# Kernel tuning notes

Measured on AMD Instinct MI355X. Metric: run time of the kernel, lower is better.

Reference implementation:

```python
import jax, jax.numpy as jnp
import numpy as np

N, E, F_IN, H, EDIM, L, OUT = 100000, 1600000, 256, 128, 16, 3, 64


def setup_inputs() -> dict:
    key = jax.random.key(0)
    ks = jax.random.split(key, 12)
    s = lambda k, shape: jax.random.normal(k, shape, jnp.float32) * 0.05
    return dict(
        x=jax.random.normal(ks[0], (N, F_IN), jnp.float32),
        edge_index=jax.random.randint(ks[1], (2, E), 0, N, jnp.int32),
        edge_attr=jax.random.normal(ks[2], (E, EDIM), jnp.float32),
        in_w=s(ks[3], (F_IN, H)), in_b=jnp.zeros((H,), jnp.float32),
        Wk=s(ks[4], (L, H, H)), bk=jnp.zeros((L, H), jnp.float32),
        Wq=s(ks[5], (L, H, H)), bq=jnp.zeros((L, H), jnp.float32),
        Wv=s(ks[6], (L, H, H)), bv=jnp.zeros((L, H), jnp.float32),
        We=s(ks[7], (L, EDIM, H)), be=jnp.zeros((L, H), jnp.float32),
        Ws=s(ks[8], (L, H, H)), bs=jnp.zeros((L, H), jnp.float32),
        ln_g=jnp.ones((L, H), jnp.float32), ln_b=jnp.zeros((L, H), jnp.float32),
        out_w=s(ks[9], (H, OUT)),
    )


def _layernorm(x, g, b, eps=1e-5):
    mu = x.mean(-1, keepdims=True)
    var = ((x - mu) ** 2).mean(-1, keepdims=True)
    return (x - mu) * jax.lax.rsqrt(var + eps) * g + b


def reference(x, edge_index, edge_attr, in_w, in_b, Wk, bk, Wq, bq, Wv, bv,
              We, be, Ws, bs, ln_g, ln_b, out_w):
    src, dst = edge_index[0], edge_index[1]  # j (source), i (target)
    h = x @ in_w + in_b                      # in_proj; dropout_prob=0 -> identity
    n = h.shape[0]
    n_layers = Wk.shape[0]
    for l in range(n_layers):
        # ResGatedGraphConv: out_i = W_skip x_i + sum_j sigmoid(k_i + e_ij + q_j) * v_j
        k = h @ Wk[l] + bk[l]                # keys on targets  [N,H]
        q = h @ Wq[l] + bq[l]                # queries on sources [N,H]
        v = h @ Wv[l] + bv[l]                # values on sources [N,H]
        e = edge_attr @ We[l] + be[l]        # edge embedding [E,H]
        gate = jax.nn.sigmoid(k[dst] + e + q[src])   # [E,H]
        msg = gate * v[src]                  # [E,H]
        agg = jax.ops.segment_sum(msg, dst, num_segments=n)  # scatter-add [N,H]
        h = agg + (h @ Ws[l] + bs[l])        # root/skip term
        h = jax.nn.gelu(_layernorm(h, ln_g[l], ln_b[l]), approximate=False)
    return h @ out_w                          # out_proj (bias=False)
```

## Files before the change

kernel.cpp:

```cpp
#include <hip/hip_runtime.h>
#include <hip/hip_fp16.h>
#include <cmath>

#define Nn   100000
#define Ee   1600000
#define FIN  256
#define Hh   128
#define EDIMM 16
#define NL   3
#define NOUT 64

typedef _Float16 f16x8 __attribute__((ext_vector_type(8)));
typedef float f32x4 __attribute__((ext_vector_type(4)));

static __device__ __forceinline__ __half2 u2h2(unsigned int u) {
  union { unsigned int u; __half2 h; } c; c.u = u; return c.h;
}
static __device__ __forceinline__ unsigned int h22u(__half2 h) {
  union { unsigned int u; __half2 h; } c; c.h = h; return c.u;
}

__global__ __launch_bounds__(128) void in_proj_kernel(const float* __restrict__ x,
    const float* __restrict__ w, const float* __restrict__ b, __half* __restrict__ h) {
  __shared__ float xs[8][FIN];
  int r0 = blockIdx.x * 8;
  for (int i = threadIdx.x; i < 8 * FIN; i += 128) {
    int r = i >> 8, c = i & (FIN - 1);
    int rr = r0 + r;
    xs[r][c] = (rr < Nn) ? x[rr * FIN + c] : 0.f;
  }
  __syncthreads();
  int t = threadIdx.x;
  float acc[8] = {};
  for (int kk = 0; kk < FIN; kk++) {
    float wv = w[kk * Hh + t];
#pragma unroll
    for (int r = 0; r < 8; r++) acc[r] += xs[r][kk] * wv;
  }
  float bias = b[t];
#pragma unroll
  for (int r = 0; r < 8; r++) {
    int rr = r0 + r;
    if (rr < Nn) h[rr * Hh + t] = __float2half(acc[r] + bias);
  }
}

__global__ __launch_bounds__(256) void prep_weights_kernel(const float* __restrict__ Wk,
    const float* __restrict__ Wq, const float* __restrict__ Wv, const float* __restrict__ Ws,
    __half* __restrict__ WtT) {
  int mat = blockIdx.x, l = blockIdx.y;
  const float* W = (mat == 0 ? Wk : mat == 1 ? Wq : mat == 2 ? Wv : Ws) + (size_t)l * Hh * Hh;
  __half* out = WtT + ((size_t)(l * 4 + mat)) * Hh * Hh;
  for (int i = threadIdx.x; i < Hh * Hh; i += 256) {
    int k = i >> 7, n = i & 127;
    out[(size_t)n * Hh + k] = __float2half(W[i]);
  }
}

__global__ __launch_bounds__(256) void kqvs_mfma_kernel(
    const __half* __restrict__ h, const __half* __restrict__ WtT_l,
    const float* __restrict__ bk, const float* __restrict__ bq,
    const float* __restrict__ bv, const float* __restrict__ bs,
    __half* __restrict__ kb, __half* __restrict__ qvj, __half* __restrict__ hnew) {
  __shared__ __half Wl[128][136];
  __shared__ __half Ht[32][136];
  int mat = blockIdx.x;
  int r0 = blockIdx.y * 32;
  int tid = threadIdx.x;

  const uint4* wg = (const uint4*)(WtT_l + (size_t)mat * Hh * Hh);
  for (int i = tid; i < 2048; i += 256) {
    int rw = i >> 4, cw = i & 15;
    *(uint4*)(&Wl[rw][cw * 8]) = wg[i];
  }
  const uint4* hg = (const uint4*)(h + (size_t)r0 * Hh);
  for (int i = tid; i < 512; i += 256) {
    int rh = i >> 4, ch = i & 15;
    *(uint4*)(&Ht[rh][ch * 8]) = hg[i];
  }
  __syncthreads();

  int wv = tid >> 6, lane = tid & 63;
  int rowHalf = wv & 1, colHalf = wv >> 1;
  int quad = lane >> 4, l16 = lane & 15;

  f32x4 acc[4];
#pragma unroll
  for (int t = 0; t < 4; t++) acc[t] = (f32x4){0.f, 0.f, 0.f, 0.f};

#pragma unroll
  for (int kstep = 0; kstep < 4; kstep++) {
    f16x8 afrag = *(const f16x8*)(&Ht[rowHalf * 16 + l16][kstep * 32 + quad * 8]);
#pragma unroll
    for (int t = 0; t < 4; t++) {
      int n = colHalf * 64 + t * 16 + l16;
      f16x8 bfrag = *(const f16x8*)(&Wl[n][kstep * 32 + quad * 8]);
      acc[t] = __builtin_amdgcn_mfma_f32_16x16x32_f16(afrag, bfrag, acc[t], 0, 0, 0);
    }
  }

  const float* bp = (mat == 0) ? bk : (mat == 1) ? bq : (mat == 2) ? bv : bs;
#pragma unroll
  for (int t = 0; t < 4; t++) {
    int col = colHalf * 64 + t * 16 + l16;
    float bval = bp[col];
#pragma unroll
    for (int r = 0; r < 4; r++) {
      int row = r0 + rowHalf * 16 + quad * 4 + r;
      __half hv = __float2half(acc[t][r] + bval);
      if (mat == 0)       kb[(size_t)row * Hh + col] = hv;
      else if (mat == 1)  qvj[(size_t)row * 256 + (col >> 1) * 4 + (col & 1)] = hv;
      else if (mat == 2)  qvj[(size_t)row * 256 + (col >> 1) * 4 + 2 + (col & 1)] = hv;
      else                hnew[(size_t)row * Hh + col] = hv;
    }
  }
}

__global__ __launch_bounds__(256) void zero_kernel(int* __restrict__ p, int n) {
  int i = blockIdx.x * 256 + threadIdx.x;
  if (i < n) p[i] = 0;
}

__global__ __launch_bounds__(256) void hist_kernel(const int* __restrict__ ei_dst,
                                                   int* __restrict__ counts) {
  int e = blockIdx.x * 256 + threadIdx.x;
  if (e < Ee) atomicAdd(&counts[ei_dst[e]], 1);
}

__global__ __launch_bounds__(256) void scan_block_kernel(const int* __restrict__ counts,
    int* __restrict__ rowptr, int* __restrict__ bsums) {
  __shared__ int tsums[256];
  int b = blockIdx.x, t = threadIdx.x;
  int base = b * 1024 + t * 4;
  int v[4]; int s = 0;
#pragma unroll
  for (int j = 0; j < 4; j++) {
    int idx = base + j;
    v[j] = (idx < Nn) ? counts[idx] : 0;
    s += v[j];
  }
  tsums[t] = s;
  __syncthreads();
  for (int off = 1; off < 256; off <<= 1) {
    int y = (t >= off) ? tsums[t - off] : 0;
    __syncthreads();
    tsums[t] += y;
    __syncthreads();
  }
  int excl = tsums[t] - s;
#pragma unroll
  for (int j = 0; j < 4; j++) {
    int idx = base + j;
    if (idx < Nn) rowptr[idx] = excl;
    excl += v[j];
  }
  if (t == 255) bsums[b] = tsums[255];
}

__global__ __launch_bounds__(128) void scan_sums_kernel(int* __restrict__ bsums, int nb) {
  __shared__ int sh[128];
  int t = threadIdx.x;
  int v = (t < nb) ? bsums[t] : 0;
  sh[t] = v;
  __syncthreads();
  for (int off = 1; off < 128; off <<= 1) {
    int y = (t >= off) ? sh[t - off] : 0;
    __syncthreads();
    sh[t] += y;
    __syncthreads();
  }
  if (t < nb) bsums[t] = sh[t] - v;
}

__global__ __launch_bounds__(256) void finalize_rowptr_kernel(int* __restrict__ rowptr,
    const int* __restrict__ bsums, int* __restrict__ cursor) {
  int i = blockIdx.x * 256 + threadIdx.x;
  if (i < Nn) {
    int r = rowptr[i] + bsums[i >> 10];
    rowptr[i] = r;
    cursor[i] = r;
  }
  if (i == Nn) rowptr[Nn] = Ee;
}

__global__ __launch_bounds__(256) void fill_perm_kernel(const int* __restrict__ ei_src,
    const int* __restrict__ ei_dst, const float* __restrict__ ea,
    int* __restrict__ cursor, int* __restrict__ src_perm,
    unsigned int* __restrict__ ea_perm) {
  int e = blockIdx.x * 256 + threadIdx.x;
  if (e < Ee) {
    int d = ei_dst[e];
    int slot = atomicAdd(&cursor[d], 1);
    src_perm[slot] = ei_src[e];
    const float4* s = (const float4*)(ea + (size_t)e * EDIMM);
    float4 f[4] = { s[0], s[1], s[2], s[3] };
    unsigned int u[16];
#pragma unroll
    for (int j = 0; j < 4; j++) {
      u[j*4+0] = h22u(__half2half2(__float2half(f[j].x)));
      u[j*4+1] = h22u(__half2half2(__float2half(f[j].y)));
      u[j*4+2] = h22u(__half2half2(__float2half(f[j].z)));
      u[j*4+3] = h22u(__half2half2(__float2half(f[j].w)));
    }
    uint4* dp = (uint4*)(ea_perm + (size_t)slot * EDIMM);
#pragma unroll
    for (int j = 0; j < 4; j++)
      dp[j] = make_uint4(u[j*4+0], u[j*4+1], u[j*4+2], u[j*4+3]);
  }
}

#define EA_CAP 48
__global__ __launch_bounds__(256, 8) void edge_csr_kernel(
    const __half* __restrict__ kb, const __half* __restrict__ qvj,
    const int* __restrict__ src_perm, const unsigned int* __restrict__ ea_perm,
    const int* __restrict__ rowptr,
    const float* __restrict__ We_l, const float* __restrict__ be_l,
    const float* __restrict__ ln_g_l, const float* __restrict__ ln_b_l,
    __half* __restrict__ hbuf) {
  __shared__ uint4 lds_ea[4][EA_CAP * 4];
  int wave = threadIdx.x >> 6;
  int lane = threadIdx.x & 63;
  int row = blockIdx.x * 4 + wave;
  int c0 = lane * 2;

  __half2 wpk[EDIMM];
#pragma unroll
  for (int d = 0; d < EDIMM; d++) {
    float2 wv = *(const float2*)(We_l + d * Hh + c0);
    wpk[d] = __floats2half2_rn(wv.x, wv.y);
  }
  float2 bef = *(const float2*)(be_l + c0);
  __half2 bev = __floats2half2_rn(bef.x, bef.y);

  __half2 kpk = *(const __half2*)(kb + (size_t)row * Hh + c0);
  __half2 kbev = __hadd2(kpk, bev);

  float agg0 = 0.f, agg1 = 0.f;
  int beg = rowptr[row], end = rowptr[row + 1];
  int deg = end - beg;
  int nl = (deg < EA_CAP) ? deg : EA_CAP;

  char* lbase = (char*)&lds_ea[wave][0];
  {
    int row_bytes = nl << 6;
    const char* gsrc = (const char*)(ea_perm + (size_t)beg * EDIMM);
    for (int c = 0; c < row_bytes; c += 1024) {
      int o = c + lane * 16;
      if (o < row_bytes) {
        __builtin_amdgcn_global_load_lds(
            (__attribute__((address_space(1))) void*)(gsrc + o),
            (__attribute__((address_space(3))) void*)(lbase + c),
            16, 0, 0);
      }
    }
  }

  const char* qvb = (const char*)qvj;
  unsigned loff = (unsigned)(lane << 3);

  auto edge_math = [&](uint4 a0, uint4 a1, uint4 a2, uint4 a3, uint2 qv) {
    __half2 qh = u2h2(qv.x), vh = u2h2(qv.y);
    __half2 acc = kbev;
    acc = __hfma2(u2h2(a0.x), wpk[0],  acc);
    acc = __hfma2(u2h2(a0.y), wpk[1],  acc);
    acc = __hfma2(u2h2(a0.z), wpk[2],  acc);
    acc = __hfma2(u2h2(a0.w), wpk[3],  acc);
    acc = __hfma2(u2h2(a1.x), wpk[4],  acc);
    acc = __hfma2(u2h2(a1.y), wpk[5],  acc);
    acc = __hfma2(u2h2(a1.z), wpk[6],  acc);
    acc = __hfma2(u2h2(a1.w), wpk[7],  acc);
    acc = __hfma2(u2h2(a2.x), wpk[8],  acc);
    acc = __hfma2(u2h2(a2.y), wpk[9],  acc);
    acc = __hfma2(u2h2(a2.z), wpk[10], acc);
    acc = __hfma2(u2h2(a2.w), wpk[11], acc);
    acc = __hfma2(u2h2(a3.x), wpk[12], acc);
    acc = __hfma2(u2h2(a3.y), wpk[13], acc);
    acc = __hfma2(u2h2(a3.z), wpk[14], acc);
    acc = __hfma2(u2h2(a3.w), wpk[15], acc);
    __half2 pre = __hadd2(acc, qh);
    float p0 = __half2float(__low2half(pre));
    float p1 = __half2float(__high2half(pre));
    float g0 = __builtin_amdgcn_rcpf(1.f + __expf(-p0));
    float g1 = __builtin_amdgcn_rcpf(1.f + __expf(-p1));
    agg0 += g0 * __half2float(__low2half(vh));
    agg1 += g1 * __half2float(__high2half(vh));
  };

  {
    int nf = nl & ~3;
    int e = 0;
    uint2 qA0, qA1, qA2, qA3;
    if (nf) {
      int4 s4 = *(const int4*)(src_perm + beg);
      qA0 = *(const uint2*)(qvb + (((unsigned)s4.x << 9) + loff));
      qA1 = *(const uint2*)(qvb + (((unsigned)s4.y << 9) + loff));
      qA2 = *(const uint2*)(qvb + (((unsigned)s4.z << 9) + loff));
      qA3 = *(const uint2*)(qvb + (((unsigned)s4.w << 9) + loff));
    }
    asm volatile("s_waitcnt vmcnt(0)" ::: "memory");

    for (; e + 8 <= nf; e += 4) {
      int4 s4n = *(const int4*)(src_perm + beg + e + 4);
      uint2 qB0 = *(const uint2*)(qvb + (((unsigned)s4n.x << 9) + loff));
      uint2 qB1 = *(const uint2*)(qvb + (((unsigned)s4n.y << 9) + loff));
      uint2 qB2 = *(const uint2*)(qvb + (((unsigned)s4n.z << 9) + loff));
      uint2 qB3 = *(const uint2*)(qvb + (((unsigned)s4n.w << 9) + loff));
      const uint4* ee = (const uint4*)(lbase + (e << 6));
      edge_math(ee[0],  ee[1],  ee[2],  ee[3],  qA0);
      edge_math(ee[4],  ee[5],  ee[6],  ee[7],  qA1);
      edge_math(ee[8],  ee[9],  ee[10], ee[11], qA2);
      edge_math(ee[12], ee[13], ee[14], ee[15], qA3);
      qA0 = qB0; qA1 = qB1; qA2 = qB2; qA3 = qB3;
    }
    if (nf) {
      const uint4* ee = (const uint4*)(lbase + (e << 6));
      edge_math(ee[0],  ee[1],  ee[2],  ee[3],  qA0);
      edge_math(ee[4],  ee[5],  ee[6],  ee[7],  qA1);
      edge_math(ee[8],  ee[9],  ee[10], ee[11], qA2);
      edge_math(ee[12], ee[13], ee[14], ee[15], qA3);
      e += 4;
    }
    for (; e < nl; e++) {
      int src = src_perm[beg + e];
      uint2 qv = *(const uint2*)(qvb + (((unsigned)src << 9) + loff));
      const uint4* ee = (const uint4*)(lbase + (e << 6));
      edge_math(ee[0], ee[1], ee[2], ee[3], qv);
    }
    for (int eg = beg + nl; eg < end; eg++) {
      int src = src_perm[eg];
      const uint4* eb = (const uint4*)(ea_perm + (size_t)eg * EDIMM);
      uint4 a0 = eb[0], a1 = eb[1], a2 = eb[2], a3 = eb[3];
      uint2 qv = *(const uint2*)(qvb + (((unsigned)src << 9) + loff));
      edge_math(a0, a1, a2, a3, qv);
    }
  }

  __half2 hv2 = *(const __half2*)(hbuf + (size_t)row * Hh + c0);
  float y0 = __half2float(hv2.x) + agg0, y1 = __half2float(hv2.y) + agg1;
  float s = y0 + y1;
#pragma unroll
  for (int off = 32; off; off >>= 1) s += __shfl_xor(s, off);
  float mu = s * (1.f / 128.f);
  float d0 = y0 - mu, d1 = y1 - mu;
  float vv = d0 * d0 + d1 * d1;
#pragma unroll
  for (int off = 32; off; off >>= 1) vv += __shfl_xor(vv, off);
  float rstd = rsqrtf(vv * (1.f / 128.f) + 1e-5f);
  float2 lg = *(const float2*)(ln_g_l + c0);
  float2 lb = *(const float2*)(ln_b_l + c0);
  float o0 = d0 * rstd * lg.x + lb.x;
  float o1 = d1 * rstd * lg.y + lb.y;
  o0 = 0.5f * o0 * (1.f + erff(o0 * 0.70710678118654752f));
  o1 = 0.5f * o1 * (1.f + erff(o1 * 0.70710678118654752f));
  *(__half2*)(hbuf + (size_t)row * Hh + c0) = __floats2half2_rn(o0, o1);
}

__global__ __launch_bounds__(64) void out_proj_kernel(const __half* __restrict__ h,
    const float* __restrict__ w, float* __restrict__ out) {
  __shared__ float hs[16][Hh];
  int r0 = blockIdx.x * 16;
  const uint4* hg = (const uint4*)(h + (size_t)r0 * Hh);
  for (int i = threadIdx.x; i < 256; i += 64) {
    uint4 u = hg[i];
    int r = i >> 4, c = (i & 15) * 8;
    __half2 ha = u2h2(u.x), hb = u2h2(u.y), hc = u2h2(u.z), hd = u2h2(u.w);
    hs[r][c+0] = __half2float(ha.x); hs[r][c+1] = __half2float(ha.y);
    hs[r][c+2] = __half2float(hb.x); hs[r][c+3] = __half2float(hb.y);
    hs[r][c+4] = __half2float(hc.x); hs[r][c+5] = __half2float(hc.y);
    hs[r][c+6] = __half2float(hd.x); hs[r][c+7] = __half2float(hd.y);
  }
  __syncthreads();
  int t = threadIdx.x;
  float acc[16] = {};
  for (int kk = 0; kk < Hh; kk++) {
    float wv = w[kk * NOUT + t];
#pragma unroll
    for (int r = 0; r < 16; r++) acc[r] += hs[r][kk] * wv;
  }
#pragma unroll
  for (int r = 0; r < 16; r++) out[(size_t)(r0 + r) * NOUT + t] = acc[r];
}

extern "C" void kernel_launch(void* const* d_in, const int* in_sizes, int n_in,
                              void* d_out, int out_size, void* d_ws, size_t ws_size,
                              hipStream_t stream) {
  const float* x    = (const float*)d_in[0];
  const int*   ei   = (const int*)d_in[1];
  const float* ea   = (const float*)d_in[2];
  const float* in_w = (const float*)d_in[3];
  const float* in_b = (const float*)d_in[4];
  const float* Wk   = (const float*)d_in[5];
  const float* bk   = (const float*)d_in[6];
  const float* Wq   = (const float*)d_in[7];
  const float* bq   = (const float*)d_in[8];
  const float* Wv   = (const float*)d_in[9];
  const float* bv   = (const float*)d_in[10];
  const float* We   = (const float*)d_in[11];
  const float* be   = (const float*)d_in[12];
  const float* Ws   = (const float*)d_in[13];
  const float* bs   = (const float*)d_in[14];
  const float* ln_g = (const float*)d_in[15];
  const float* ln_b = (const float*)d_in[16];
  const float* out_w = (const float*)d_in[17];
  float* out = (float*)d_out;

  const int* ei_src = ei;
  const int* ei_dst = ei + Ee;

  size_t NH = (size_t)Nn * Hh;
  char* wsp = (char*)d_ws;
  __half* hA = (__half*)wsp;          wsp += NH * 2;
  __half* hB = (__half*)wsp;          wsp += NH * 2;
  __half* kb = (__half*)wsp;          wsp += NH * 2;
  __half* qvj = (__half*)wsp;         wsp += NH * 2 * 2;
  __half* WtT = (__half*)wsp;         wsp += (size_t)NL * 4 * Hh * Hh * 2;
  int* rowptr = (int*)wsp;            wsp += (Nn + 1) * 4;
  int* cursor = (int*)wsp;            wsp += Nn * 4;
  int* bsums  = (int*)wsp;            wsp += 128 * 4;
  int* src_perm = (int*)wsp;          wsp += (size_t)Ee * 4;
  unsigned int* ea_perm = (unsigned int*)wsp; wsp += (size_t)Ee * EDIMM * 4;

  const int NB_SCAN = (Nn + 1023) / 1024;

  zero_kernel<<<(Nn + 255) / 256, 256, 0, stream>>>(cursor, Nn);
  hist_kernel<<<(Ee + 255) / 256, 256, 0, stream>>>(ei_dst, cursor);
  scan_block_kernel<<<NB_SCAN, 256, 0, stream>>>(cursor, rowptr, bsums);
  scan_sums_kernel<<<1, 128, 0, stream>>>(bsums, NB_SCAN);
  finalize_rowptr_kernel<<<(Nn + 1 + 255) / 256, 256, 0, stream>>>(rowptr, bsums, cursor);
  fill_perm_kernel<<<(Ee + 255) / 256, 256, 0, stream>>>(ei_src, ei_dst, ea, cursor,
                                                         src_perm, ea_perm);
  prep_weights_kernel<<<dim3(4, NL), 256, 0, stream>>>(Wk, Wq, Wv, Ws, WtT);

  in_proj_kernel<<<(Nn + 7) / 8, 128, 0, stream>>>(x, in_w, in_b, hA);

  __half* h  = hA;
  __half* hn = hB;
  for (int l = 0; l < NL; l++) {
    kqvs_mfma_kernel<<<dim3(4, Nn / 32), 256, 0, stream>>>(h,
        WtT + (size_t)l * 4 * Hh * Hh,
        bk + l * Hh, bq + l * Hh, bv + l * Hh, bs + l * Hh,
        kb, qvj, hn);
    edge_csr_kernel<<<Nn / 4, 256, 0, stream>>>(kb, qvj, src_perm, ea_perm,
        rowptr, We + l * EDIMM * Hh, be + l * Hh,
        ln_g + l * Hh, ln_b + l * Hh, hn);
    __half* tmp = h; h = hn; hn = tmp;
  }

  out_proj_kernel<<<Nn / 16, 64, 0, stream>>>(h, out_w, out);
}
```

Measured before the change: 1.336 ms.

## Pack edge attributes as plain half2 and fold log2e into gate weights

```diff
diff --git a/kernel.cpp b/kernel.cpp
--- a/kernel.cpp
+++ b/kernel.cpp
@@ -9,6 +9,7 @@
 #define EDIMM 16
 #define NL   3
 #define NOUT 64
+#define LOG2E 1.4426950408889634f
 
 typedef _Float16 f16x8 __attribute__((ext_vector_type(8)));
 typedef float f32x4 __attribute__((ext_vector_type(4)));
@@ -19,6 +20,13 @@
 static __device__ __forceinline__ unsigned int h22u(__half2 h) {
   union { unsigned int u; __half2 h; } c; c.h = h; return c.u;
 }
+
+#define PK_FMA_LO(acc, a, w) \
+  asm("v_pk_fma_f16 %0, %1, %2, %0 op_sel:[0,0,0] op_sel_hi:[0,1,1]" \
+      : "+v"(acc) : "v"(a), "v"(w))
+#define PK_FMA_HI(acc, a, w) \
+  asm("v_pk_fma_f16 %0, %1, %2, %0 op_sel:[1,0,0] op_sel_hi:[1,1,1]" \
+      : "+v"(acc) : "v"(a), "v"(w))
 
 __global__ __launch_bounds__(128) void in_proj_kernel(const float* __restrict__ x,
     const float* __restrict__ w, const float* __restrict__ b, __half* __restrict__ h) {
@@ -50,10 +58,11 @@
     __half* __restrict__ WtT) {
   int mat = blockIdx.x, l = blockIdx.y;
   const float* W = (mat == 0 ? Wk : mat == 1 ? Wq : mat == 2 ? Wv : Ws) + (size_t)l * Hh * Hh;
+  float sc = (mat < 2) ? LOG2E : 1.f;
   __half* out = WtT + ((size_t)(l * 4 + mat)) * Hh * Hh;
   for (int i = threadIdx.x; i < Hh * Hh; i += 256) {
     int k = i >> 7, n = i & 127;
-    out[(size_t)n * Hh + k] = __float2half(W[i]);
+    out[(size_t)n * Hh + k] = __float2half(W[i] * sc);
   }
 }
 
@@ -100,10 +109,11 @@
   }
 
   const float* bp = (mat == 0) ? bk : (mat == 1) ? bq : (mat == 2) ? bv : bs;
+  float bscale = (mat < 2) ? LOG2E : 1.f;
 #pragma unroll
   for (int t = 0; t < 4; t++) {
     int col = colHalf * 64 + t * 16 + l16;
-    float bval = bp[col];
+    float bval = bp[col] * bscale;
 #pragma unroll
     for (int r = 0; r < 4; r++) {
       int row = r0 + rowHalf * 16 + quad * 4 + r;
@@ -193,47 +203,40 @@
     int slot = atomicAdd(&cursor[d], 1);
     src_perm[slot] = ei_src[e];
     const float4* s = (const float4*)(ea + (size_t)e * EDIMM);
-    float4 f[4] = { s[0], s[1], s[2], s[3] };
-    unsigned int u[16];
-#pragma unroll
-    for (int j = 0; j < 4; j++) {
-      u[j*4+0] = h22u(__half2half2(__float2half(f[j].x)));
-      u[j*4+1] = h22u(__half2half2(__float2half(f[j].y)));
-      u[j*4+2] = h22u(__half2half2(__float2half(f[j].z)));
-      u[j*4+3] = h22u(__half2half2(__float2half(f[j].w)));
-    }
-    uint4* dp = (uint4*)(ea_perm + (size_t)slot * EDIMM);
-#pragma unroll
-    for (int j = 0; j < 4; j++)
-      dp[j] = make_uint4(u[j*4+0], u[j*4+1], u[j*4+2], u[j*4+3]);
+    float4 f0 = s[0], f1 = s[1], f2 = s[2], f3 = s[3];
+    uint4* dp = (uint4*)(ea_perm + (size_t)slot * 8);
+    dp[0] = make_uint4(h22u(__floats2half2_rn(f0.x, f0.y)), h22u(__floats2half2_rn(f0.z, f0.w)),
+                       h22u(__floats2half2_rn(f1.x, f1.y)), h22u(__floats2half2_rn(f1.z, f1.w)));
+    dp[1] = make_uint4(h22u(__floats2half2_rn(f2.x, f2.y)), h22u(__floats2half2_rn(f2.z, f2.w)),
+                       h22u(__floats2half2_rn(f3.x, f3.y)), h22u(__floats2half2_rn(f3.z, f3.w)));
   }
 }
 
 #define EA_CAP 48
-__global__ __launch_bounds__(256, 8) void edge_csr_kernel(
+__global__ __launch_bounds__(256, 6) void edge_csr_kernel(
     const __half* __restrict__ kb, const __half* __restrict__ qvj,
     const int* __restrict__ src_perm, const unsigned int* __restrict__ ea_perm,
     const int* __restrict__ rowptr,
     const float* __restrict__ We_l, const float* __restrict__ be_l,
     const float* __restrict__ ln_g_l, const float* __restrict__ ln_b_l,
     __half* __restrict__ hbuf) {
-  __shared__ uint4 lds_ea[4][EA_CAP * 4];
+  __shared__ uint4 lds_ea[4][EA_CAP * 2];
   int wave = threadIdx.x >> 6;
   int lane = threadIdx.x & 63;
   int row = blockIdx.x * 4 + wave;
   int c0 = lane * 2;
 
-  __half2 wpk[EDIMM];
+  unsigned wpk[EDIMM];
 #pragma unroll
   for (int d = 0; d < EDIMM; d++) {
     float2 wv = *(const float2*)(We_l + d * Hh + c0);
-    wpk[d] = __floats2half2_rn(wv.x, wv.y);
+    wpk[d] = h22u(__floats2half2_rn(wv.x * LOG2E, wv.y * LOG2E));
   }
   float2 bef = *(const float2*)(be_l + c0);
-  __half2 bev = __floats2half2_rn(bef.x, bef.y);
+  __half2 bev = __floats2half2_rn(bef.x * LOG2E, bef.y * LOG2E);
 
   __half2 kpk = *(const __half2*)(kb + (size_t)row * Hh + c0);
-  __half2 kbev = __hadd2(kpk, bev);
+  unsigned kbev_u = h22u(__hadd2(kpk, bev));
 
   float agg0 = 0.f, agg1 = 0.f;
   int beg = rowptr[row], end = rowptr[row + 1];
@@ -242,8 +245,8 @@
 
   char* lbase = (char*)&lds_ea[wave][0];
   {
-    int row_bytes = nl << 6;
-    const char* gsrc = (const char*)(ea_perm + (size_t)beg * EDIMM);
+    int row_bytes = nl << 5;
+    const char* gsrc = (const char*)(ea_perm + (size_t)beg * 8);
     for (int c = 0; c < row_bytes; c += 1024) {
       int o = c + lane * 16;
       if (o < row_bytes) {
@@ -258,30 +261,25 @@
   const char* qvb = (const char*)qvj;
   unsigned loff = (unsigned)(lane << 3);
 
-  auto edge_math = [&](uint4 a0, uint4 a1, uint4 a2, uint4 a3, uint2 qv) {
-    __half2 qh = u2h2(qv.x), vh = u2h2(qv.y);
-    __half2 acc = kbev;
-    acc = __hfma2(u2h2(a0.x), wpk[0],  acc);
-    acc = __hfma2(u2h2(a0.y), wpk[1],  acc);
-    acc = __hfma2(u2h2(a0.z), wpk[2],  acc);
-    acc = __hfma2(u2h2(a0.w), wpk[3],  acc);
-    acc = __hfma2(u2h2(a1.x), wpk[4],  acc);
-    acc = __hfma2(u2h2(a1.y), wpk[5],  acc);
-    acc = __hfma2(u2h2(a1.z), wpk[6],  acc);
-    acc = __hfma2(u2h2(a1.w), wpk[7],  acc);
-    acc = __hfma2(u2h2(a2.x), wpk[8],  acc);
-    acc = __hfma2(u2h2(a2.y), wpk[9],  acc);
-    acc = __hfma2(u2h2(a2.z), wpk[10], acc);
-    acc = __hfma2(u2h2(a2.w), wpk[11], acc);
-    acc = __hfma2(u2h2(a3.x), wpk[12], acc);
-    acc = __hfma2(u2h2(a3.y), wpk[13], acc);
-    acc = __hfma2(u2h2(a3.z), wpk[14], acc);
-    acc = __hfma2(u2h2(a3.w), wpk[15], acc);
-    __half2 pre = __hadd2(acc, qh);
+  auto edge_math = [&](uint4 eA, uint4 eB, uint2 qv) {
+    unsigned acc = kbev_u;
+    PK_FMA_LO(acc, eA.x, wpk[0]);  PK_FMA_HI(acc, eA.x, wpk[1]);
+    PK_FMA_LO(acc, eA.y, wpk[2]);  PK_FMA_HI(acc, eA.y, wpk[3]);
+    PK_FMA_LO(acc, eA.z, wpk[4]);  PK_FMA_HI(acc, eA.z, wpk[5]);
+    PK_FMA_LO(acc, eA.w, wpk[6]);  PK_FMA_HI(acc, eA.w, wpk[7]);
+    PK_FMA_LO(acc, eB.x, wpk[8]);  PK_FMA_HI(acc, eB.x, wpk[9]);
+    PK_FMA_LO(acc, eB.y, wpk[10]); PK_FMA_HI(acc, eB.y, wpk[11]);
+    PK_FMA_LO(acc, eB.z, wpk[12]); PK_FMA_HI(acc, eB.z, wpk[13]);
+    PK_FMA_LO(acc, eB.w, wpk[14]); PK_FMA_HI(acc, eB.w, wpk[15]);
+    __half2 pre = __hadd2(u2h2(acc), u2h2(qv.x));
     float p0 = __half2float(__low2half(pre));
     float p1 = __half2float(__high2half(pre));
-    float g0 = __builtin_amdgcn_rcpf(1.f + __expf(-p0));
-    float g1 = __builtin_amdgcn_rcpf(1.f + __expf(-p1));
+    float ex0, ex1;
+    asm("v_exp_f32 %0, -%1" : "=v"(ex0) : "v"(p0));
+    asm("v_exp_f32 %0, -%1" : "=v"(ex1) : "v"(p1));
+    float g0 = __builtin_amdgcn_rcpf(1.f + ex0);
+    float g1 = __builtin_amdgcn_rcpf(1.f + ex1);
+    __half2 vh = u2h2(qv.y);
     agg0 += g0 * __half2float(__low2half(vh));
     agg1 += g1 * __half2float(__high2half(vh));
   };
@@ -305,33 +303,33 @@
       uint2 qB1 = *(const uint2*)(qvb + (((unsigned)s4n.y << 9) + loff));
       uint2 qB2 = *(const uint2*)(qvb + (((unsigned)s4n.z << 9) + loff));
       uint2 qB3 = *(const uint2*)(qvb + (((unsigned)s4n.w << 9) + loff));
-      const uint4* ee = (const uint4*)(lbase + (e << 6));
-      edge_math(ee[0],  ee[1],  ee[2],  ee[3],  qA0);
-      edge_math(ee[4],  ee[5],  ee[6],  ee[7],  qA1);
-      edge_math(ee[8],  ee[9],  ee[10], ee[11], qA2);
-      edge_math(ee[12], ee[13], ee[14], ee[15], qA3);
+      const uint4* ee = (const uint4*)(lbase + (e << 5));
+      edge_math(ee[0], ee[1], qA0);
+      edge_math(ee[2], ee[3], qA1);
+      edge_math(ee[4], ee[5], qA2);
+      edge_math(ee[6], ee[7], qA3);
       qA0 = qB0; qA1 = qB1; qA2 = qB2; qA3 = qB3;
     }
     if (nf) {
-      const uint4* ee = (const uint4*)(lbase + (e << 6));
-      edge_math(ee[0],  ee[1],  ee[2],  ee[3],  qA0);
-      edge_math(ee[4],  ee[5],  ee[6],  ee[7],  qA1);
-      edge_math(ee[8],  ee[9],  ee[10], ee[11], qA2);
-      edge_math(ee[12], ee[13], ee[14], ee[15], qA3);
+      const uint4* ee = (const uint4*)(lbase + (e << 5));
+      edge_math(ee[0], ee[1], qA0);
+      edge_math(ee[2], ee[3], qA1);
+      edge_math(ee[4], ee[5], qA2);
+      edge_math(ee[6], ee[7], qA3);
       e += 4;
     }
     for (; e < nl; e++) {
       int src = src_perm[beg + e];
       uint2 qv = *(const uint2*)(qvb + (((unsigned)src << 9) + loff));
-      const uint4* ee = (const uint4*)(lbase + (e << 6));
-      edge_math(ee[0], ee[1], ee[2], ee[3], qv);
+      const uint4* ee = (const uint4*)(lbase + (e << 5));
+      edge_math(ee[0], ee[1], qv);
     }
     for (int eg = beg + nl; eg < end; eg++) {
       int src = src_perm[eg];
-      const uint4* eb = (const uint4*)(ea_perm + (size_t)eg * EDIMM);
-      uint4 a0 = eb[0], a1 = eb[1], a2 = eb[2], a3 = eb[3];
+      const uint4* eb = (const uint4*)(ea_perm + (size_t)eg * 8);
+      uint4 a0 = eb[0], a1 = eb[1];
       uint2 qv = *(const uint2*)(qvb + (((unsigned)src << 9) + loff));
-      edge_math(a0, a1, a2, a3, qv);
+      edge_math(a0, a1, qv);
     }
   }
 
@@ -418,7 +416,7 @@
   int* cursor = (int*)wsp;            wsp += Nn * 4;
   int* bsums  = (int*)wsp;            wsp += 128 * 4;
   int* src_perm = (int*)wsp;          wsp += (size_t)Ee * 4;
-  unsigned int* ea_perm = (unsigned int*)wsp; wsp += (size_t)Ee * EDIMM * 4;
+  unsigned int* ea_perm = (unsigned int*)wsp; wsp += (size_t)Ee * 32;
 
   const int NB_SCAN = (Nn + 1023) / 1024;
 
```

Result: faster. 1.268 ms (-5.1%).
